# Optimization experiments

Hardware: AMD Instinct MI355X
Metric: run time of the kernel (lower is better)

The kernel has to match this reference:

```python
import jax, jax.numpy as jnp
import numpy as np

ALPHA = 0.25
GAMMA = 2.0
W_CLASS = W_BBOX = W_GIOU = W_MASK = W_DICE = W_PROJ = 1.0
EPS = 1e-8


def box_cxcywh_to_xyxy(b):
    cx, cy, w, h = jnp.split(b, 4, axis=-1)
    return jnp.concatenate([cx - 0.5 * w, cy - 0.5 * h, cx + 0.5 * w, cy + 0.5 * h], axis=-1)


def dice_coef(inputs, targets):
    # inputs: logits [N, D]; targets: binary [M, D]
    s = jax.nn.sigmoid(inputs)
    num = 2.0 * jnp.einsum('nd,md->nm', s, targets)
    den = s.sum(-1)[:, None] + targets.sum(-1)[None, :]
    return (num + 1.0) / (den + 1.0)  # [N, M]


def sigmoid_focal_coef(inputs, targets):
    # inputs: logits [N, D]; targets: binary [M, D] -> [N, M]
    x = inputs[:, None, :]
    t = targets[None, :, :]
    p = jax.nn.sigmoid(x)
    # BCE-with-logits, numerically stable
    ce = jnp.maximum(x, 0.0) - x * t + jnp.log1p(jnp.exp(-jnp.abs(x)))
    p_t = p * t + (1.0 - p) * (1.0 - t)
    alpha_t = ALPHA * t + (1.0 - ALPHA) * (1.0 - t)
    return (alpha_t * ce * (1.0 - p_t) ** GAMMA).mean(-1)


def giou_cost(src_xyxy, tgt_xyxy):
    # src [nf, nq, 4], tgt [nf, 1, 4] -> cost [nf, nq, 1]
    a1 = (src_xyxy[..., 2] - src_xyxy[..., 0]) * (src_xyxy[..., 3] - src_xyxy[..., 1])
    a2 = (tgt_xyxy[..., 2] - tgt_xyxy[..., 0]) * (tgt_xyxy[..., 3] - tgt_xyxy[..., 1])
    lt = jnp.maximum(src_xyxy[:, :, None, :2], tgt_xyxy[:, None, :, :2])
    rb = jnp.minimum(src_xyxy[:, :, None, 2:], tgt_xyxy[:, None, :, 2:])
    wh = jnp.clip(rb - lt, 0.0)
    inter = wh[..., 0] * wh[..., 1]
    union = a1[:, :, None] + a2[:, None, :] - inter
    iou = inter / union
    ltc = jnp.minimum(src_xyxy[:, :, None, :2], tgt_xyxy[:, None, :, :2])
    rbc = jnp.maximum(src_xyxy[:, :, None, 2:], tgt_xyxy[:, None, :, 2:])
    whc = jnp.clip(rbc - ltc, 0.0)
    areac = whc[..., 0] * whc[..., 1]
    giou = iou - (areac - union) / areac
    return -giou


def cost_matrix_one(logits, boxes, masks, tmask, tbox, tvalid):
    # logits [nf,nq,1], boxes [nf,nq,4], masks [nf,nq,H,W], tmask [nf,H,W], tbox [nf,4], tvalid [nf]
    p = jax.nn.sigmoid(logits[..., 0])  # [nf, nq]
    neg = (1.0 - ALPHA) * p ** GAMMA * (-jnp.log(1.0 - p + EPS))
    pos = ALPHA * (1.0 - p) ** GAMMA * (-jnp.log(p + EPS))
    w = (tvalid != 0).astype(p.dtype)  # valid-frame mask replaces python `continue`
    cost_class = (((pos - neg) * w[:, None]).sum(0) / w.sum())[:, None]  # [nq, 1]

    cost_bbox = jnp.abs(boxes[:, :, None, :] - tbox[:, None, None, :]).sum(-1).mean(0)  # [nq, 1]
    cost_giou = giou_cost(box_cxcywh_to_xyxy(boxes), box_cxcywh_to_xyxy(tbox[:, None, :])).mean(0)

    out_mask = jnp.transpose(masks, (1, 0, 2, 3))  # [nq, nf, H, W]
    nq = out_mask.shape[0]
    flat_src = out_mask.reshape(nq, -1)
    flat_tgt = tmask.reshape(1, -1)
    cost_mask = sigmoid_focal_coef(flat_src, flat_tgt)  # [nq, 1]
    cost_dice = -dice_coef(flat_src, flat_tgt)

    src_y = jnp.max(out_mask, axis=2, keepdims=True).reshape(nq, -1)  # [nq, nf*W]
    src_x = jnp.max(out_mask, axis=3, keepdims=True).reshape(nq, -1)  # [nq, nf*H]
    tgt_y = jnp.max(tmask[None], axis=2, keepdims=True).reshape(1, -1)
    tgt_x = jnp.max(tmask[None], axis=3, keepdims=True).reshape(1, -1)
    cost_proj = -0.5 * (dice_coef(src_y, tgt_y) + dice_coef(src_x, tgt_x))

    C = (W_CLASS * cost_class + W_BBOX * cost_bbox + W_GIOU * cost_giou
         + W_MASK * cost_mask + W_DICE * cost_dice + W_PROJ * cost_proj)
    return C  # [nq, 1]


def setup_inputs() -> dict:
    key = jax.random.key(0)
    k = jax.random.split(key, 6)
    bs, nf, nq, H, W = 2, 8, 300, 96, 96
    pred_logits = jax.random.normal(k[0], (bs, nf, nq, 1), dtype=jnp.float32)
    pred_boxes = jax.random.uniform(k[1], (bs, nf, nq, 4), dtype=jnp.float32)
    pred_masks = jax.random.normal(k[2], (bs, nf, nq, H, W), dtype=jnp.float32)
    target_masks = (jax.random.uniform(k[3], (bs, nf, H, W)) < 0.3).astype(jnp.float32)
    tgt_boxes = jax.random.uniform(k[4], (bs, nf, 4), dtype=jnp.float32)
    tgt_valid = jnp.ones((bs, nf), dtype=jnp.int32)
    valid_pad = jnp.zeros((bs, H, W), dtype=bool)
    return {"pred_logits": pred_logits, "pred_boxes": pred_boxes, "pred_masks": pred_masks,
            "target_masks": target_masks, "tgt_boxes": tgt_boxes, "tgt_valid": tgt_valid,
            "valid_pad": valid_pad}


def reference(pred_logits, pred_boxes, pred_masks, target_masks, tgt_boxes, tgt_valid, valid_pad):
    # zero out predictions over padded regions (masked_fill with valid[:, None, None])
    masks = jnp.where(valid_pad[:, None, None, :, :], 0.0, pred_masks)
    C = jax.vmap(cost_matrix_one)(pred_logits, pred_boxes, masks, target_masks, tgt_boxes, tgt_valid)
    src_ind = jnp.argmin(C, axis=1).astype(jnp.int64)  # [bs, 1]
    tgt_ind = jnp.zeros_like(src_ind)
    return C, src_ind, tgt_ind
```

## Files before the change

kernel.cpp:

```cpp
#include <hip/hip_runtime.h>
#include <math.h>

#define NF 8
#define NQ 300
#define HSZ 96
#define WSZ 96
#define HW (HSZ*WSZ)
#define DTOT (NF*HW)
#define NBF 16

#define WS_TGTY  0
#define WS_TGTX  1536
#define WS_TSUM  3072
#define WS_YSUM  3088
#define WS_XSUM  3104
#define WS_TBITS 3136
#define WS_PBITS 7744
#define WS_PART  8320

__device__ __forceinline__ float sigmoid_fast(float x) {
    float e = __expf(-fabsf(x));
    float inv = __builtin_amdgcn_rcpf(1.f + e);
    return x >= 0.f ? inv : e * inv;
}

#define NTT 1024
__global__ __launch_bounds__(NTT)
void targets_kernel(const float* __restrict__ tm, const unsigned char* __restrict__ vpad,
                    float* __restrict__ ws) {
    int bf = blockIdx.x, t = threadIdx.x;
    int lane = t & 63, wid = t >> 6;
    __shared__ float tile[HSZ * 97];
    __shared__ float redt[16 * 3];
    const float* base = tm + (size_t)bf * HW;
    unsigned* tbw = (unsigned*)(ws + WS_TBITS) + bf * 288;

    float tsum = 0.f;
    #pragma unroll
    for (int it = 0; it < 9; ++it) {
        int e = it * NTT + t;
        float v = base[e];
        tsum += v;
        tile[e + e / 96] = v;
        unsigned long long m = __ballot(v != 0.f);
        int word = it * 32 + wid * 2;
        if (lane == 0)       tbw[word]     = (unsigned)m;
        else if (lane == 32) tbw[word + 1] = (unsigned)(m >> 32);
    }
    if ((bf & 7) == 0) {
        const unsigned char* vb = vpad + (size_t)(bf >> 3) * HW;
        unsigned* pbw = (unsigned*)(ws + WS_PBITS) + (bf >> 3) * 288;
        #pragma unroll
        for (int it = 0; it < 9; ++it) {
            int e = it * NTT + t;
            unsigned long long m = __ballot(vb[e] != 0);
            int word = it * 32 + wid * 2;
            if (lane == 0)       pbw[word]     = (unsigned)m;
            else if (lane == 32) pbw[word + 1] = (unsigned)(m >> 32);
        }
    }
    __syncthreads();

    float ysum = 0.f, xsum = 0.f;
    if (t < 96) {
        float m = -INFINITY;
        #pragma unroll 8
        for (int h = 0; h < HSZ; ++h) m = fmaxf(m, tile[h * 97 + t]);
        ws[WS_TGTY + bf * 96 + t] = m;
        ysum = m;
    } else if (t < 192) {
        int hh = t - 96;
        float m = -INFINITY;
        #pragma unroll 8
        for (int w = 0; w < WSZ; ++w) m = fmaxf(m, tile[hh * 97 + w]);
        ws[WS_TGTX + bf * 96 + hh] = m;
        xsum = m;
    }
    float s0 = tsum, s1 = ysum, s2 = xsum;
    #pragma unroll
    for (int off = 32; off > 0; off >>= 1) {
        s0 += __shfl_down(s0, off, 64);
        s1 += __shfl_down(s1, off, 64);
        s2 += __shfl_down(s2, off, 64);
    }
    if (lane == 0) { redt[wid * 3] = s0; redt[wid * 3 + 1] = s1; redt[wid * 3 + 2] = s2; }
    __syncthreads();
    if (t == 0) {
        float a0 = 0.f, a1 = 0.f, a2 = 0.f;
        #pragma unroll
        for (int w = 0; w < 16; ++w) {
            a0 += redt[w * 3]; a1 += redt[w * 3 + 1]; a2 += redt[w * 3 + 2];
        }
        ws[WS_TSUM + bf] = a0;
        ws[WS_YSUM + bf] = a1;
        ws[WS_XSUM + bf] = a2;
    }
}

#define NTP 384
__global__ __launch_bounds__(NTP, 6)
void partial_kernel(const float* __restrict__ masks, const float* __restrict__ ws,
                    float* __restrict__ part) {
    int bid = blockIdx.x;
    int bf = bid / NQ;
    int q  = bid - bf * NQ;
    int b  = bf >> 3, f = bf & 7;
    int t  = threadIdx.x;
    int w4 = t % 24;
    int r0 = t / 24;
    int wsh = (t & 7) * 4;

    __shared__ float rp[96 * 25];
    __shared__ float cp[16 * 100];
    __shared__ float red[6][8];

    const float4* mrow = (const float4*)(masks + (size_t)bid * HW);
    const unsigned* tbw = (const unsigned*)(ws + WS_TBITS) + bf * 288;
    const unsigned* pbw = (const unsigned*)(ws + WS_PBITS) + b * 288;

    float4 xv[6];
    unsigned tw[6], pw[6];
    #pragma unroll
    for (int k = 0; k < 6; ++k) xv[k] = mrow[k * NTP + t];
    #pragma unroll
    for (int k = 0; k < 6; ++k) tw[k] = tbw[k * 48 + (t >> 3)];
    #pragma unroll
    for (int k = 0; k < 6; ++k) pw[k] = pbw[k * 48 + (t >> 3)];

    float focal = 0.f, dnum = 0.f, dden = 0.f;
    float cm0 = -INFINITY, cm1 = -INFINITY, cm2 = -INFINITY, cm3 = -INFINITY;

    #pragma unroll
    for (int k = 0; k < 6; ++k) {
        unsigned tn = (tw[k] >> wsh) & 0xFu;
        unsigned pn = (pw[k] >> wsh) & 0xFu;
        float xs[4] = {xv[k].x, xv[k].y, xv[k].z, xv[k].w};
        if (pn) {
            #pragma unroll
            for (int j = 0; j < 4; ++j) if ((pn >> j) & 1u) xs[j] = 0.f;
        }
        float rmx = -INFINITY;
        #pragma unroll
        for (int j = 0; j < 4; ++j) {
            float x = xs[j];
            float tg = (float)((tn >> j) & 1u);
            float e = __expf(-fabsf(x));
            float se = 1.f + e;
            float inv = __builtin_amdgcn_rcpf(se);
            float s = x >= 0.f ? inv : e * inv;
            float L = __logf(se);
            float ce = fmaf(-x, tg, fmaxf(x, 0.f) + L);
            float omp = fmaf(tg, fmaf(-2.f, s, 1.f), s);
            float at = fmaf(tg, -0.5f, 0.75f);
            focal = fmaf(at * ce, omp * omp, focal);
            dnum = fmaf(s, tg, dnum);
            dden += s;
            rmx = fmaxf(rmx, x);
        }
        cm0 = fmaxf(cm0, xs[0]); cm1 = fmaxf(cm1, xs[1]);
        cm2 = fmaxf(cm2, xs[2]); cm3 = fmaxf(cm3, xs[3]);
        rp[(16 * k + r0) * 25 + w4] = rmx;
    }
    {
        float4 cmv = {cm0, cm1, cm2, cm3};
        *(float4*)&cp[r0 * 100 + w4 * 4] = cmv;
    }
    __syncthreads();

    float v0 = focal, v1 = dnum, v2 = dden, v3 = 0.f, v4 = 0.f, v5 = 0.f, v6 = 0.f;
    if (t < 96) {
        float m = -INFINITY;
        #pragma unroll
        for (int p = 0; p < 16; ++p) m = fmaxf(m, cp[p * 100 + t]);
        float sg = sigmoid_fast(m);
        v4 = sg;
        v3 = sg * ws[WS_TGTY + bf * 96 + t];
    } else if (t < 192) {
        int r = t - 96;
        float m = rp[r * 25];
        #pragma unroll
        for (int c = 1; c < 24; ++c) m = fmaxf(m, rp[r * 25 + c]);
        float sg = sigmoid_fast(m);
        v6 = sg;
        v5 = sg * ws[WS_TGTX + bf * 96 + r];
    }
    #pragma unroll
    for (int off = 32; off > 0; off >>= 1) {
        v0 += __shfl_down(v0, off, 64);
        v1 += __shfl_down(v1, off, 64);
        v2 += __shfl_down(v2, off, 64);
        v3 += __shfl_down(v3, off, 64);
        v4 += __shfl_down(v4, off, 64);
        v5 += __shfl_down(v5, off, 64);
        v6 += __shfl_down(v6, off, 64);
    }
    int wid = t >> 6, lane = t & 63;
    if (lane == 0) {
        red[wid][0] = v0; red[wid][1] = v1; red[wid][2] = v2; red[wid][3] = v3;
        red[wid][4] = v4; red[wid][5] = v5; red[wid][6] = v6;
    }
    __syncthreads();
    if (t == 0) {
        float* o = part + (size_t)((b * NQ + q) * NF + f) * 8;
        #pragma unroll
        for (int i = 0; i < 7; ++i)
            o[i] = red[0][i] + red[1][i] + red[2][i] + red[3][i] + red[4][i] + red[5][i];
    }
}

#define NTC 64
__global__ __launch_bounds__(NTC)
void combine_kernel(const float* __restrict__ logits, const float* __restrict__ boxes,
                    const float* __restrict__ tbox, const int* __restrict__ tvalid,
                    const float* __restrict__ ws, float* __restrict__ out) {
    int gid = blockIdx.x * NTC + threadIdx.x;
    if (gid >= 2 * NQ) return;
    int b = gid / NQ, q = gid - b * NQ;

    const float* pbase = ws + WS_PART + (size_t)gid * (NF * 8);
    float focal = 0.f, dnum = 0.f, dden = 0.f;
    float pYn = 0.f, pYd = 0.f, pXn = 0.f, pXd = 0.f;
    float tsum = 0.f, ysum = 0.f, xsum = 0.f;
    #pragma unroll
    for (int f = 0; f < NF; ++f) {
        int bf = b * NF + f;
        const float* p = pbase + f * 8;
        focal += p[0]; dnum += p[1]; dden += p[2];
        pYn += p[3]; pYd += p[4]; pXn += p[5]; pXd += p[6];
        tsum += ws[WS_TSUM + bf];
        ysum += ws[WS_YSUM + bf];
        xsum += ws[WS_XSUM + bf];
    }
    float cost_mask = focal / (float)DTOT;
    float cost_dice = -(2.f * dnum + 1.f) / (dden + tsum + 1.f);
    float coefY = (2.f * pYn + 1.f) / (pYd + ysum + 1.f);
    float coefX = (2.f * pXn + 1.f) / (pXd + xsum + 1.f);
    float cost_proj = -0.5f * (coefY + coefX);

    float wsum = 0.f, cls = 0.f, cb = 0.f, cg = 0.f;
    #pragma unroll
    for (int f = 0; f < NF; ++f) {
        float wv = (tvalid[b * NF + f] != 0) ? 1.f : 0.f;
        wsum += wv;
        float lg = logits[(b * NF + f) * NQ + q];
        float p = sigmoid_fast(lg);
        float negc = 0.75f * p * p * (-__logf(1.f - p + 1e-8f));
        float posc = 0.25f * (1.f - p) * (1.f - p) * (-__logf(p + 1e-8f));
        cls += (posc - negc) * wv;

        const float* bx = boxes + (size_t)((b * NF + f) * NQ + q) * 4;
        const float* tb = tbox + (b * NF + f) * 4;
        float cx = bx[0], cy = bx[1], bw = bx[2], bh = bx[3];
        float tcx = tb[0], tcy = tb[1], tbw = tb[2], tbh = tb[3];
        cb += fabsf(cx - tcx) + fabsf(cy - tcy) + fabsf(bw - tbw) + fabsf(bh - tbh);
        float sx1 = cx - 0.5f * bw, sy1 = cy - 0.5f * bh;
        float sx2 = cx + 0.5f * bw, sy2 = cy + 0.5f * bh;
        float tx1 = tcx - 0.5f * tbw, ty1 = tcy - 0.5f * tbh;
        float tx2 = tcx + 0.5f * tbw, ty2 = tcy + 0.5f * tbh;
        float a1 = (sx2 - sx1) * (sy2 - sy1), a2 = (tx2 - tx1) * (ty2 - ty1);
        float iw = fmaxf(fminf(sx2, tx2) - fmaxf(sx1, tx1), 0.f);
        float ih = fmaxf(fminf(sy2, ty2) - fmaxf(sy1, ty1), 0.f);
        float inter = iw * ih;
        float uni = a1 + a2 - inter;
        float iou = inter / uni;
        float cw = fmaxf(fmaxf(sx2, tx2) - fminf(sx1, tx1), 0.f);
        float chh = fmaxf(fmaxf(sy2, ty2) - fminf(sy1, ty1), 0.f);
        float areac = cw * chh;
        cg += -(iou - (areac - uni) / areac);
    }
    cls /= wsum;
    cb *= 0.125f;
    cg *= 0.125f;
    out[b * NQ + q] = cls + cb + cg + cost_mask + cost_dice + cost_proj;
}

#define NT 256
__global__ __launch_bounds__(NT)
void argmin_kernel(float* __restrict__ out, int write_idx) {
    int b = blockIdx.x, t = threadIdx.x;
    float best = INFINITY;
    int bi = 0x7fffffff;
    for (int q = t; q < NQ; q += NT) {
        float v = out[b * NQ + q];
        if (v < best) { best = v; bi = q; }
    }
    #pragma unroll
    for (int off = 32; off > 0; off >>= 1) {
        float ov = __shfl_down(best, off, 64);
        int oi = __shfl_down(bi, off, 64);
        if (ov < best || (ov == best && oi < bi)) { best = ov; bi = oi; }
    }
    __shared__ float rv[4];
    __shared__ int ri[4];
    int wid = t >> 6, lane = t & 63;
    if (lane == 0) { rv[wid] = best; ri[wid] = bi; }
    __syncthreads();
    if (t == 0 && write_idx) {
        #pragma unroll
        for (int w = 1; w < 4; ++w) {
            if (rv[w] < best || (rv[w] == best && ri[w] < bi)) { best = rv[w]; bi = ri[w]; }
        }
        out[2 * NQ + b] = (float)bi;
        out[2 * NQ + 2 + b] = 0.f;
    }
}

extern "C" void kernel_launch(void* const* d_in, const int* in_sizes, int n_in,
                              void* d_out, int out_size, void* d_ws, size_t ws_size,
                              hipStream_t stream) {
    const float* logits = (const float*)d_in[0];
    const float* boxes  = (const float*)d_in[1];
    const float* masks  = (const float*)d_in[2];
    const float* tmask  = (const float*)d_in[3];
    const float* tbox   = (const float*)d_in[4];
    const int*   tvalid = (const int*)d_in[5];
    const unsigned char* vpad = (const unsigned char*)d_in[6];
    float* out = (float*)d_out;
    float* ws  = (float*)d_ws;

    targets_kernel<<<NBF, NTT, 0, stream>>>(tmask, vpad, ws);
    partial_kernel<<<NBF * NQ, NTP, 0, stream>>>(masks, ws, ws + WS_PART);
    combine_kernel<<<(2 * NQ + NTC - 1) / NTC, NTC, 0, stream>>>(logits, boxes, tbox,
                                                                 tvalid, ws, out);
    int write_idx = (out_size >= 2 * NQ + 4) ? 1 : 0;
    argmin_kernel<<<2, NT, 0, stream>>>(out, write_idx);
}
```

Baseline: 284.1 us.

## Process four queries per block with register double-buffered mask prefetch

Each partial_kernel block now handles four consecutive queries of one batch-frame instead of one. Target and pad bit words and the per-row/column target weights are loaded once and reused across the four queries. The next query's mask tile is prefetched into a second register buffer while the current one is processed. Barriers become explicit lgkmcnt waits plus s_barrier, and launch bounds drop from 6 to 4 blocks per CU to make room for the extra registers. The grid shrinks fourfold, which lowers occupancy and may cause tail imbalance across CUs.

```diff
diff --git a/kernel.cpp b/kernel.cpp
--- a/kernel.cpp
+++ b/kernel.cpp
@@ -98,113 +98,135 @@
 }
 
 #define NTP 384
-__global__ __launch_bounds__(NTP, 6)
+#define QPB 4
+__global__ __launch_bounds__(NTP, 4)
 void partial_kernel(const float* __restrict__ masks, const float* __restrict__ ws,
                     float* __restrict__ part) {
     int bid = blockIdx.x;
-    int bf = bid / NQ;
-    int q  = bid - bf * NQ;
-    int b  = bf >> 3, f = bf & 7;
-    int t  = threadIdx.x;
-    int w4 = t % 24;
-    int r0 = t / 24;
+    int bf  = bid / (NQ / QPB);
+    int q0  = (bid - bf * (NQ / QPB)) * QPB;
+    int b   = bf >> 3, f = bf & 7;
+    int t   = threadIdx.x;
+    int w4  = t % 24;
+    int r0  = t / 24;
     int wsh = (t & 7) * 4;
 
     __shared__ float rp[96 * 25];
     __shared__ float cp[16 * 100];
     __shared__ float red[6][8];
 
-    const float4* mrow = (const float4*)(masks + (size_t)bid * HW);
     const unsigned* tbw = (const unsigned*)(ws + WS_TBITS) + bf * 288;
     const unsigned* pbw = (const unsigned*)(ws + WS_PBITS) + b * 288;
 
-    float4 xv[6];
     unsigned tw[6], pw[6];
     #pragma unroll
-    for (int k = 0; k < 6; ++k) xv[k] = mrow[k * NTP + t];
-    #pragma unroll
     for (int k = 0; k < 6; ++k) tw[k] = tbw[k * 48 + (t >> 3)];
     #pragma unroll
     for (int k = 0; k < 6; ++k) pw[k] = pbw[k * 48 + (t >> 3)];
-
-    float focal = 0.f, dnum = 0.f, dden = 0.f;
-    float cm0 = -INFINITY, cm1 = -INFINITY, cm2 = -INFINITY, cm3 = -INFINITY;
-
-    #pragma unroll
-    for (int k = 0; k < 6; ++k) {
-        unsigned tn = (tw[k] >> wsh) & 0xFu;
-        unsigned pn = (pw[k] >> wsh) & 0xFu;
-        float xs[4] = {xv[k].x, xv[k].y, xv[k].z, xv[k].w};
-        if (pn) {
-            #pragma unroll
-            for (int j = 0; j < 4; ++j) if ((pn >> j) & 1u) xs[j] = 0.f;
-        }
-        float rmx = -INFINITY;
-        #pragma unroll
-        for (int j = 0; j < 4; ++j) {
-            float x = xs[j];
-            float tg = (float)((tn >> j) & 1u);
-            float e = __expf(-fabsf(x));
-            float se = 1.f + e;
-            float inv = __builtin_amdgcn_rcpf(se);
-            float s = x >= 0.f ? inv : e * inv;
-            float L = __logf(se);
-            float ce = fmaf(-x, tg, fmaxf(x, 0.f) + L);
-            float omp = fmaf(tg, fmaf(-2.f, s, 1.f), s);
-            float at = fmaf(tg, -0.5f, 0.75f);
-            focal = fmaf(at * ce, omp * omp, focal);
-            dnum = fmaf(s, tg, dnum);
-            dden += s;
-            rmx = fmaxf(rmx, x);
-        }
-        cm0 = fmaxf(cm0, xs[0]); cm1 = fmaxf(cm1, xs[1]);
-        cm2 = fmaxf(cm2, xs[2]); cm3 = fmaxf(cm3, xs[3]);
-        rp[(16 * k + r0) * 25 + w4] = rmx;
-    }
-    {
-        float4 cmv = {cm0, cm1, cm2, cm3};
-        *(float4*)&cp[r0 * 100 + w4 * 4] = cmv;
-    }
-    __syncthreads();
-
-    float v0 = focal, v1 = dnum, v2 = dden, v3 = 0.f, v4 = 0.f, v5 = 0.f, v6 = 0.f;
-    if (t < 96) {
-        float m = -INFINITY;
-        #pragma unroll
-        for (int p = 0; p < 16; ++p) m = fmaxf(m, cp[p * 100 + t]);
-        float sg = sigmoid_fast(m);
-        v4 = sg;
-        v3 = sg * ws[WS_TGTY + bf * 96 + t];
-    } else if (t < 192) {
-        int r = t - 96;
-        float m = rp[r * 25];
-        #pragma unroll
-        for (int c = 1; c < 24; ++c) m = fmaxf(m, rp[r * 25 + c]);
-        float sg = sigmoid_fast(m);
-        v6 = sg;
-        v5 = sg * ws[WS_TGTX + bf * 96 + r];
-    }
-    #pragma unroll
-    for (int off = 32; off > 0; off >>= 1) {
-        v0 += __shfl_down(v0, off, 64);
-        v1 += __shfl_down(v1, off, 64);
-        v2 += __shfl_down(v2, off, 64);
-        v3 += __shfl_down(v3, off, 64);
-        v4 += __shfl_down(v4, off, 64);
-        v5 += __shfl_down(v5, off, 64);
-        v6 += __shfl_down(v6, off, 64);
-    }
-    int wid = t >> 6, lane = t & 63;
-    if (lane == 0) {
-        red[wid][0] = v0; red[wid][1] = v1; red[wid][2] = v2; red[wid][3] = v3;
-        red[wid][4] = v4; red[wid][5] = v5; red[wid][6] = v6;
-    }
-    __syncthreads();
-    if (t == 0) {
-        float* o = part + (size_t)((b * NQ + q) * NF + f) * 8;
-        #pragma unroll
-        for (int i = 0; i < 7; ++i)
-            o[i] = red[0][i] + red[1][i] + red[2][i] + red[3][i] + red[4][i] + red[5][i];
+    float gy = 0.f, gx = 0.f;
+    if (t < 96)       gy = ws[WS_TGTY + bf * 96 + t];
+    else if (t < 192) gx = ws[WS_TGTX + bf * 96 + (t - 96)];
+
+    const float4* mrow = (const float4*)(masks + (size_t)(bf * NQ + q0) * HW);
+
+    float4 xa[6], xb[6];
+    #pragma unroll
+    for (int k = 0; k < 6; ++k) xa[k] = mrow[k * NTP + t];
+
+    #pragma unroll
+    for (int i = 0; i < QPB; ++i) {
+        if (i + 1 < QPB) {
+            const float4* mnext = mrow + (size_t)(i + 1) * (HW / 4);
+            #pragma unroll
+            for (int k = 0; k < 6; ++k) xb[k] = mnext[k * NTP + t];
+        }
+
+        float focal = 0.f, dnum = 0.f, dden = 0.f;
+        float cm0 = -INFINITY, cm1 = -INFINITY, cm2 = -INFINITY, cm3 = -INFINITY;
+
+        #pragma unroll
+        for (int k = 0; k < 6; ++k) {
+            unsigned tn = (tw[k] >> wsh) & 0xFu;
+            unsigned pn = (pw[k] >> wsh) & 0xFu;
+            float xs[4] = {xa[k].x, xa[k].y, xa[k].z, xa[k].w};
+            if (pn) {
+                #pragma unroll
+                for (int j = 0; j < 4; ++j) if ((pn >> j) & 1u) xs[j] = 0.f;
+            }
+            float rmx = -INFINITY;
+            #pragma unroll
+            for (int j = 0; j < 4; ++j) {
+                float x = xs[j];
+                float tg = (float)((tn >> j) & 1u);
+                float e = __expf(-fabsf(x));
+                float se = 1.f + e;
+                float inv = __builtin_amdgcn_rcpf(se);
+                float s = x >= 0.f ? inv : e * inv;
+                float L = __logf(se);
+                float ce = fmaf(-x, tg, fmaxf(x, 0.f) + L);
+                float omp = fmaf(tg, fmaf(-2.f, s, 1.f), s);
+                float at = fmaf(tg, -0.5f, 0.75f);
+                focal = fmaf(at * ce, omp * omp, focal);
+                dnum = fmaf(s, tg, dnum);
+                dden += s;
+                rmx = fmaxf(rmx, x);
+            }
+            cm0 = fmaxf(cm0, xs[0]); cm1 = fmaxf(cm1, xs[1]);
+            cm2 = fmaxf(cm2, xs[2]); cm3 = fmaxf(cm3, xs[3]);
+            rp[(16 * k + r0) * 25 + w4] = rmx;
+        }
+        {
+            float4 cmv = {cm0, cm1, cm2, cm3};
+            *(float4*)&cp[r0 * 100 + w4 * 4] = cmv;
+        }
+        asm volatile("s_waitcnt lgkmcnt(0)" ::: "memory");
+        __builtin_amdgcn_s_barrier();
+
+        float v0 = focal, v1 = dnum, v2 = dden, v3 = 0.f, v4 = 0.f, v5 = 0.f, v6 = 0.f;
+        if (t < 96) {
+            float m = -INFINITY;
+            #pragma unroll
+            for (int p = 0; p < 16; ++p) m = fmaxf(m, cp[p * 100 + t]);
+            float sg = sigmoid_fast(m);
+            v4 = sg;
+            v3 = sg * gy;
+        } else if (t < 192) {
+            int r = t - 96;
+            float m = rp[r * 25];
+            #pragma unroll
+            for (int c = 1; c < 24; ++c) m = fmaxf(m, rp[r * 25 + c]);
+            float sg = sigmoid_fast(m);
+            v6 = sg;
+            v5 = sg * gx;
+        }
+        #pragma unroll
+        for (int off = 32; off > 0; off >>= 1) {
+            v0 += __shfl_down(v0, off, 64);
+            v1 += __shfl_down(v1, off, 64);
+            v2 += __shfl_down(v2, off, 64);
+            v3 += __shfl_down(v3, off, 64);
+            v4 += __shfl_down(v4, off, 64);
+            v5 += __shfl_down(v5, off, 64);
+            v6 += __shfl_down(v6, off, 64);
+        }
+        int wid = t >> 6, lane = t & 63;
+        if (lane == 0) {
+            red[wid][0] = v0; red[wid][1] = v1; red[wid][2] = v2; red[wid][3] = v3;
+            red[wid][4] = v4; red[wid][5] = v5; red[wid][6] = v6;
+        }
+        asm volatile("s_waitcnt lgkmcnt(0)" ::: "memory");
+        __builtin_amdgcn_s_barrier();
+        if (t == 0) {
+            float* o = part + (size_t)((b * NQ + q0 + i) * NF + f) * 8;
+            #pragma unroll
+            for (int ii = 0; ii < 7; ++ii)
+                o[ii] = red[0][ii] + red[1][ii] + red[2][ii] + red[3][ii] + red[4][ii] + red[5][ii];
+        }
+
+        if (i + 1 < QPB) {
+            #pragma unroll
+            for (int k = 0; k < 6; ++k) xa[k] = xb[k];
+        }
     }
 }
 
@@ -319,7 +341,7 @@
     float* ws  = (float*)d_ws;
 
     targets_kernel<<<NBF, NTT, 0, stream>>>(tmask, vpad, ws);
-    partial_kernel<<<NBF * NQ, NTP, 0, stream>>>(masks, ws, ws + WS_PART);
+    partial_kernel<<<NBF * (NQ / QPB), NTP, 0, stream>>>(masks, ws, ws + WS_PART);
     combine_kernel<<<(2 * NQ + NTC - 1) / NTC, NTC, 0, stream>>>(logits, boxes, tbox,
                                                                  tvalid, ws, out);
     int write_idx = (out_size >= 2 * NQ + 4) ? 1 : 0;
```

After: 349.8 us. +23.1%, slower.
